# Kernel tuning notes

Measured on AMD Instinct MI355X. Metric: run time of the kernel, lower is better.

Reference implementation:

```python
import jax, jax.numpy as jnp
import numpy as np


def _bilinear_zeros(yb, ix, iy):
    # yb: [C,H,W]; ix, iy: [D,H,W] pixel coords (align_corners=False convention)
    # zeros padding: each corner masked individually, matching F.grid_sample
    h, w = yb.shape[1], yb.shape[2]
    x0 = jnp.floor(ix)
    y0 = jnp.floor(iy)
    wx = ix - x0  # [D,H,W]
    wy = iy - y0
    x0i = x0.astype(jnp.int32)
    y0i = y0.astype(jnp.int32)
    x1i = x0i + 1
    y1i = y0i + 1

    def gather(yi, xi):
        m = ((xi >= 0) & (xi < w) & (yi >= 0) & (yi < h)).astype(yb.dtype)
        yc = jnp.clip(yi, 0, h - 1)
        xc = jnp.clip(xi, 0, w - 1)
        return yb[:, yc, xc] * m[None]  # [C,D,H,W]

    v00 = gather(y0i, x0i)
    v01 = gather(y0i, x1i)
    v10 = gather(y1i, x0i)
    v11 = gather(y1i, x1i)
    wx = wx[None]
    wy = wy[None]
    return (v00 * (1 - wx) * (1 - wy) + v01 * wx * (1 - wy)
            + v10 * (1 - wx) * wy + v11 * wx * wy)


def cost_volume(x, y, disp_range_samples, ndisp):
    bs, c, h, w = x.shape
    dt = x.dtype
    mw = jnp.arange(w, dtype=dt)  # [W]
    mh = jnp.arange(h, dtype=dt)  # [H]
    # normalized grid coords as in the torch module (align_corners=True style normalize)
    cur_x = mw[None, None, None, :] - disp_range_samples  # [B,D,H,W]
    gx = cur_x / ((w - 1.0) / 2.0) - 1.0
    gy = mh / ((h - 1.0) / 2.0) - 1.0  # [H]
    # F.grid_sample default align_corners=False unnormalization
    ix = ((gx + 1.0) * w - 1.0) * 0.5  # [B,D,H,W]
    iy = ((gy + 1.0) * h - 1.0) * 0.5  # [H]
    iy_full = jnp.broadcast_to(iy[None, None, :, None], ix.shape)
    warped = jax.vmap(_bilinear_zeros)(y, ix, iy_full)  # [B,C,D,H,W]
    left = jnp.broadcast_to(x[:, :, None, :, :], (bs, c, ndisp, h, w))
    return jnp.concatenate([left, warped], axis=1)  # [B,2C,D,H,W]


def setup_inputs() -> dict:
    key = jax.random.key(0)
    k1, k2, k3 = jax.random.split(key, 3)
    B, C, H, W, D = 1, 32, 128, 256, 48
    x = jax.random.normal(k1, (B, C, H, W), dtype=jnp.float32)
    y = jax.random.normal(k2, (B, C, H, W), dtype=jnp.float32)
    disp = jax.random.uniform(k3, (B, D, H, W), dtype=jnp.float32) * 64.0
    return {"x": x, "y": y, "disp_range_samples": disp, "ndisp": D}


def reference(x, y, disp_range_samples, ndisp):
    return cost_volume(x, y, disp_range_samples, ndisp)
```

## Files before the change

kernel.cpp:

```cpp
#include <hip/hip_runtime.h>


typedef float v4f __attribute__((ext_vector_type(4)));

namespace {
constexpr int C = 32, D = 48, H = 128, W = 256;
constexpr int HW  = H * W;
constexpr int DHW = D * HW;
constexpr int TW   = 64;
constexpr int SPAN = 132;
constexpr int CP   = 36;
constexpr int NPAR = D * TW;
}

__global__ __launch_bounds__(256, 2) void cost_volume_kernel(
    const float* __restrict__ x, const float* __restrict__ y,
    const float* __restrict__ disp, float* __restrict__ out)
{
    __shared__ __align__(16) float ys[2 * SPAN * CP];
    __shared__ float s_wx[NPAR];
    __shared__ int   s_xj[NPAR];

    const int t  = threadIdx.x;
    const int bx = blockIdx.x;
    const int h  = bx >> 2;
    const int w0 = (bx & 3) * TW;
    const int xlo = w0 - 66;

    for (int id = t; id < NPAR; id += 256) {
        const int d = id >> 6, w = id & 63;
        const float dv = disp[d * HW + h * W + w0 + w];
        const float cur_x = (float)(w0 + w) - dv;
        const float gx = cur_x / 127.5f - 1.0f;
        const float ix = ((gx + 1.0f) * 256.0f - 1.0f) * 0.5f;
        const float x0f = floorf(ix);
        s_wx[id] = ix - x0f;
        const int j = (int)x0f - xlo;
        s_xj[id] = min(max(j, 0), SPAN - 2);
    }

    const float gy  = (float)h / 63.5f - 1.0f;
    const float iy  = ((gy + 1.0f) * 128.0f - 1.0f) * 0.5f;
    const float y0f = floorf(iy);
    const float wy  = iy - y0f;
    const int   y0i = (int)y0f;

    {
        const int seg = t >> 2;
        const int row = seg >> 5;
        const int cc  = seg & 31;
        const int yr  = y0i + row;
        const bool vr = (yr >= 0) && (yr < H);
        const float* ysrc = y + cc * HW + yr * W;
        for (int j = (t & 3); j < SPAN; j += 4) {
            const int xg = xlo + j;
            float v = 0.0f;
            if (vr && xg >= 0 && xg < W) v = ysrc[xg];
            ys[(row * SPAN + j) * CP + cc] = v;
        }
    }
    __syncthreads();

    const int wq = t & 15;
    const int cq = (t >> 4) & 7;
    const int d0 = t >> 7;
    const int c0 = cq * 4;
    const int wb = wq * 4;

    v4f xv[4];
#pragma unroll
    for (int cc = 0; cc < 4; ++cc)
        xv[cc] = *(const v4f*)(x + (c0 + cc) * HW + h * W + w0 + wb);

    const float omy = 1.0f - wy;
    float* const outL = out + h * W + w0 + wb;

    for (int i = 0; i < 24; ++i) {
        const int d = d0 + 2 * i;
        const int pid = d * TW + wb;
        float res[4][4];
#pragma unroll
        for (int k = 0; k < 4; ++k) {
            const float wx = s_wx[pid + k];
            const int   j  = s_xj[pid + k];
            const float omx = 1.0f - wx;
            const float w00 = omx * omy, w01 = wx * omy;
            const float w10 = omx * wy,  w11 = wx * wy;
            const float* p0 = ys + j * CP + c0;
            const float* p1 = p0 + SPAN * CP;
            const v4f v00 = *(const v4f*)p0;
            const v4f v01 = *(const v4f*)(p0 + CP);
            const v4f v10 = *(const v4f*)p1;
            const v4f v11 = *(const v4f*)(p1 + CP);
#pragma unroll
            for (int cc = 0; cc < 4; ++cc)
                res[cc][k] = fmaf(v11[cc], w11, fmaf(v10[cc], w10,
                              fmaf(v01[cc], w01, v00[cc] * w00)));
        }
        float* const ob = outL + d * HW;
#pragma unroll
        for (int cc = 0; cc < 4; ++cc) {
            const v4f r = { res[cc][0], res[cc][1], res[cc][2], res[cc][3] };
            __builtin_nontemporal_store(xv[cc], (v4f*)(ob + (c0 + cc) * DHW));
            __builtin_nontemporal_store(r, (v4f*)(ob + (C + c0 + cc) * DHW));
        }
    }
}

extern "C" void kernel_launch(void* const* d_in, const int* in_sizes, int n_in,
                              void* d_out, int out_size, void* d_ws, size_t ws_size,
                              hipStream_t stream) {
    const float* x    = (const float*)d_in[0];
    const float* y    = (const float*)d_in[1];
    const float* disp = (const float*)d_in[2];
    float* out = (float*)d_out;

    cost_volume_kernel<<<dim3(H * (W / TW)), dim3(256), 0, stream>>>(x, y, disp, out);
}
```

Before: 421.3 us.

## Repartition blocks by row, channel half and disparity half with full-width tiles

Each block now covers a full image row and splits work by half the channels and half the disparities, instead of a 64-wide column tile over all channels and disparities. The shared-memory staging of per-pixel weights is dropped; each thread computes its own bilinear weights from a vectorized disparity load. The left-feature broadcast is written in a separate loop after the warped writes. The intent is to get larger contiguous store streams and less shared-memory traffic per block, in exchange for staging a wider y span that is reloaded by the two disparity-half blocks of each row.

```diff
diff --git a/kernel.cpp b/kernel.cpp
--- a/kernel.cpp
+++ b/kernel.cpp
@@ -7,37 +7,24 @@
 constexpr int C = 32, D = 48, H = 128, W = 256;
 constexpr int HW  = H * W;
 constexpr int DHW = D * HW;
-constexpr int TW   = 64;
-constexpr int SPAN = 132;
-constexpr int CP   = 36;
-constexpr int NPAR = D * TW;
+constexpr int SPAN = 324;
+constexpr int XLO  = -66;
+constexpr int CP   = 20;
 }
 
-__global__ __launch_bounds__(256, 2) void cost_volume_kernel(
+__global__ __launch_bounds__(512, 4) void cost_volume_kernel(
     const float* __restrict__ x, const float* __restrict__ y,
     const float* __restrict__ disp, float* __restrict__ out)
 {
     __shared__ __align__(16) float ys[2 * SPAN * CP];
-    __shared__ float s_wx[NPAR];
-    __shared__ int   s_xj[NPAR];
 
-    const int t  = threadIdx.x;
-    const int bx = blockIdx.x;
-    const int h  = bx >> 2;
-    const int w0 = (bx & 3) * TW;
-    const int xlo = w0 - 66;
-
-    for (int id = t; id < NPAR; id += 256) {
-        const int d = id >> 6, w = id & 63;
-        const float dv = disp[d * HW + h * W + w0 + w];
-        const float cur_x = (float)(w0 + w) - dv;
-        const float gx = cur_x / 127.5f - 1.0f;
-        const float ix = ((gx + 1.0f) * 256.0f - 1.0f) * 0.5f;
-        const float x0f = floorf(ix);
-        s_wx[id] = ix - x0f;
-        const int j = (int)x0f - xlo;
-        s_xj[id] = min(max(j, 0), SPAN - 2);
-    }
+    const int t     = threadIdx.x;
+    const int bx    = blockIdx.x;
+    const int h     = bx >> 2;
+    const int ch    = (bx >> 1) & 1;
+    const int dh    = bx & 1;
+    const int cb    = ch * 16;
+    const int dbase = dh * 24;
 
     const float gy  = (float)h / 63.5f - 1.0f;
     const float iy  = ((gy + 1.0f) * 128.0f - 1.0f) * 0.5f;
@@ -46,63 +33,79 @@
     const int   y0i = (int)y0f;
 
     {
-        const int seg = t >> 2;
-        const int row = seg >> 5;
-        const int cc  = seg & 31;
+        const int combo = t >> 4;
+        const int row = combo >> 4;
+        const int cc  = combo & 15;
         const int yr  = y0i + row;
         const bool vr = (yr >= 0) && (yr < H);
-        const float* ysrc = y + cc * HW + yr * W;
-        for (int j = (t & 3); j < SPAN; j += 4) {
-            const int xg = xlo + j;
+        const float* ysrc = y + (cb + cc) * HW + yr * W;
+        for (int j = (t & 15); j < SPAN; j += 16) {
+            const int xg = XLO + j;
             float v = 0.0f;
             if (vr && xg >= 0 && xg < W) v = ysrc[xg];
             ys[(row * SPAN + j) * CP + cc] = v;
         }
     }
+
+    const int wave = t >> 6;
+    const int lane = t & 63;
+    const int w0   = 4 * lane;
+
+    v4f xv0 = *(const v4f*)(x + (cb + wave * 2 + 0) * HW + h * W + w0);
+    v4f xv1 = *(const v4f*)(x + (cb + wave * 2 + 1) * HW + h * W + w0);
+
     __syncthreads();
 
-    const int wq = t & 15;
-    const int cq = (t >> 4) & 7;
-    const int d0 = t >> 7;
-    const int c0 = cq * 4;
-    const int wb = wq * 4;
+    const float omy = 1.0f - wy;
+    float* const outw = out + (C + cb) * DHW + h * W + w0;
 
-    v4f xv[4];
-#pragma unroll
-    for (int cc = 0; cc < 4; ++cc)
-        xv[cc] = *(const v4f*)(x + (c0 + cc) * HW + h * W + w0 + wb);
-
-    const float omy = 1.0f - wy;
-    float* const outL = out + h * W + w0 + wb;
-
-    for (int i = 0; i < 24; ++i) {
-        const int d = d0 + 2 * i;
-        const int pid = d * TW + wb;
-        float res[4][4];
+    for (int dd = 0; dd < 3; ++dd) {
+        const int d = dbase + wave * 3 + dd;
+        const v4f dv = *(const v4f*)(disp + d * HW + h * W + w0);
+        float wgt[4][4]; int jj[4];
 #pragma unroll
         for (int k = 0; k < 4; ++k) {
-            const float wx = s_wx[pid + k];
-            const int   j  = s_xj[pid + k];
+            const float cur = (float)(w0 + k) - dv[k];
+            const float gx  = cur / 127.5f - 1.0f;
+            const float ix  = ((gx + 1.0f) * 256.0f - 1.0f) * 0.5f;
+            const float x0f = floorf(ix);
+            const float wx  = ix - x0f;
+            jj[k] = min(max((int)x0f - XLO, 0), SPAN - 2);
             const float omx = 1.0f - wx;
-            const float w00 = omx * omy, w01 = wx * omy;
-            const float w10 = omx * wy,  w11 = wx * wy;
-            const float* p0 = ys + j * CP + c0;
-            const float* p1 = p0 + SPAN * CP;
-            const v4f v00 = *(const v4f*)p0;
-            const v4f v01 = *(const v4f*)(p0 + CP);
-            const v4f v10 = *(const v4f*)p1;
-            const v4f v11 = *(const v4f*)(p1 + CP);
+            wgt[k][0] = omx * omy; wgt[k][1] = wx * omy;
+            wgt[k][2] = omx * wy;  wgt[k][3] = wx * wy;
+        }
 #pragma unroll
-            for (int cc = 0; cc < 4; ++cc)
-                res[cc][k] = fmaf(v11[cc], w11, fmaf(v10[cc], w10,
-                              fmaf(v01[cc], w01, v00[cc] * w00)));
+        for (int cq = 0; cq < 4; ++cq) {
+            const int c0 = cq * 4;
+            float res[4][4];
+#pragma unroll
+            for (int k = 0; k < 4; ++k) {
+                const float* p0 = ys + jj[k] * CP + c0;
+                const float* p1 = p0 + SPAN * CP;
+                const v4f v00 = *(const v4f*)p0;
+                const v4f v01 = *(const v4f*)(p0 + CP);
+                const v4f v10 = *(const v4f*)p1;
+                const v4f v11 = *(const v4f*)(p1 + CP);
+#pragma unroll
+                for (int cc = 0; cc < 4; ++cc)
+                    res[cc][k] = fmaf(v11[cc], wgt[k][3], fmaf(v10[cc], wgt[k][2],
+                                  fmaf(v01[cc], wgt[k][1], v00[cc] * wgt[k][0])));
+            }
+#pragma unroll
+            for (int cc = 0; cc < 4; ++cc) {
+                const v4f r = { res[cc][0], res[cc][1], res[cc][2], res[cc][3] };
+                __builtin_nontemporal_store(r, (v4f*)(outw + (c0 + cc) * DHW + d * HW));
+            }
         }
-        float* const ob = outL + d * HW;
-#pragma unroll
-        for (int cc = 0; cc < 4; ++cc) {
-            const v4f r = { res[cc][0], res[cc][1], res[cc][2], res[cc][3] };
-            __builtin_nontemporal_store(xv[cc], (v4f*)(ob + (c0 + cc) * DHW));
-            __builtin_nontemporal_store(r, (v4f*)(ob + (C + c0 + cc) * DHW));
+    }
+
+    {
+        float* op0 = out + (cb + wave * 2 + 0) * DHW + dbase * HW + h * W + w0;
+        float* op1 = out + (cb + wave * 2 + 1) * DHW + dbase * HW + h * W + w0;
+        for (int d = 0; d < 24; ++d) {
+            __builtin_nontemporal_store(xv0, (v4f*)(op0 + d * HW));
+            __builtin_nontemporal_store(xv1, (v4f*)(op1 + d * HW));
         }
     }
 }
@@ -115,5 +118,5 @@
     const float* disp = (const float*)d_in[2];
     float* out = (float*)d_out;
 
-    cost_volume_kernel<<<dim3(H * (W / TW)), dim3(256), 0, stream>>>(x, y, disp, out);
+    cost_volume_kernel<<<dim3(512), dim3(512), 0, stream>>>(x, y, disp, out);
 }
```

Result: no change. 418.8 us (-0.6%).
